# Performance work log

Hardware: AMD Instinct MI355X
Metric: run time of the kernel (lower is better)

Reference implementation:

```python
import jax, jax.numpy as jnp
import numpy as np
from jax import lax

DIM = 256
NH = 16          # num_heads; head_dim = DIM//NH == NH (required by scale broadcast)
HD = DIM // NH   # 16
HID = int(DIM * 1.0)  # mlp hidden (ffn_expansion_factor=1.0)
B, H, W = 4, 128, 128
EPS = 1e-5


def _conv(x, w, pad, groups=1):
    # x: NCHW, w: OIHW
    return lax.conv_general_dilated(x, w, (1, 1), [(pad, pad), (pad, pad)],
                                    dimension_numbers=('NCHW', 'OIHW', 'NCHW'),
                                    feature_group_count=groups)


def _ln(x, w, b):
    # WithBias LayerNorm over channel axis (torch does it in b,(hw),c layout -> axis=c)
    mu = x.mean(1, keepdims=True)
    var = ((x - mu) ** 2).mean(1, keepdims=True)
    return (x - mu) / jnp.sqrt(var + EPS) * w[None, :, None, None] + b[None, :, None, None]


def setup_inputs() -> dict:
    key = jax.random.key(0)
    ks = jax.random.split(key, 12)
    s = 0.02
    return {
        'x': jax.random.normal(ks[0], (B, DIM, H, W), jnp.float32),
        'ln1_w': jnp.ones((DIM,), jnp.float32),
        'ln1_b': jnp.zeros((DIM,), jnp.float32),
        'conv3_w': jax.random.normal(ks[1], (DIM, 1, 3, 3), jnp.float32) * s,
        'conv3_b': jnp.zeros((DIM,), jnp.float32),
        'conv5_w': jax.random.normal(ks[2], (DIM, 1, 5, 5), jnp.float32) * s,
        'conv5_b': jnp.zeros((DIM,), jnp.float32),
        'qkv_w': jax.random.normal(ks[3], (3 * DIM, DIM), jnp.float32) * s,  # 1x1 conv, no bias
        'scale': jnp.ones((NH, 1, 1), jnp.float32),
        'g1_w': jax.random.normal(ks[4], (DIM // 4, DIM), jnp.float32) * s,
        'g1_b': jnp.zeros((DIM // 4,), jnp.float32),
        'g2_w': jax.random.normal(ks[5], (2, DIM // 4), jnp.float32) * s,
        'g2_b': jnp.zeros((2,), jnp.float32),
        'proj_w': jax.random.normal(ks[6], (DIM, DIM), jnp.float32) * s,
        'proj_b': jnp.zeros((DIM,), jnp.float32),
        'ln2_w': jnp.ones((DIM,), jnp.float32),
        'ln2_b': jnp.zeros((DIM,), jnp.float32),
        'pin_w': jax.random.normal(ks[7], (2 * HID, DIM), jnp.float32) * s,  # 1x1, bias=False
        'dw_w': jax.random.normal(ks[8], (2 * HID, 2, 3, 3), jnp.float32) * s,  # groups=HID
        'pout_w': jax.random.normal(ks[9], (DIM, HID), jnp.float32) * s,
    }


def _forward(x, ln1_w, ln1_b, conv3_w, conv3_b, conv5_w, conv5_b, qkv_w, scale,
             g1_w, g1_b, g2_w, g2_b, proj_w, proj_b, ln2_w, ln2_b, pin_w, dw_w, pout_w):
    b, c, h, w = x.shape
    # ---- token mixer (CAFormer) ----
    y = _ln(x, ln1_w, ln1_b)
    conv_feat = (_conv(y, conv3_w, 1, groups=DIM) + conv3_b[None, :, None, None]
                 + _conv(y, conv5_w, 2, groups=DIM) + conv5_b[None, :, None, None])
    qkv = jnp.einsum('oc,bchw->bohw', qkv_w, y)  # (b, 3c, h, w)
    q, k, v = jnp.split(qkv.reshape(b, 3, NH, HD, h * w), 3, axis=1)
    q, k, v = q[:, 0], k[:, 0], v[:, 0]  # (b, nh, hd, h*w)
    # L2 normalize over entire flattened spatial extent (F.normalize, eps=1e-12)
    q = q / jnp.maximum(jnp.linalg.norm(q, axis=-1, keepdims=True), 1e-12)
    k = k / jnp.maximum(jnp.linalg.norm(k, axis=-1, keepdims=True), 1e-12)
    q4 = q.reshape(b, NH, HD, h, w)
    k4 = k.reshape(b, NH, HD, h, w)
    v4 = v.reshape(b, NH, HD, h, w)
    # scale (nh,1,1) right-aligned against (b,nh,hd,x,x): broadcasts along hd axis
    sc = scale.reshape(1, 1, NH, 1, 1)
    # horizontal (row) attention: per (b,head,hd-channel), rows attend to rows
    attn_h = jax.nn.softmax(jnp.einsum('bhdxy,bhdzy->bhdxz', q4, k4) * sc, axis=-1)
    out_h = jnp.einsum('bhdxz,bhdzy->bhdxy', attn_h, v4).reshape(b, c, h, w)
    # vertical (column) attention
    qt, kt, vt = (t.swapaxes(-1, -2) for t in (q4, k4, v4))  # (b,nh,hd,w,h)
    attn_v = jax.nn.softmax(jnp.einsum('bhdyx,bhdzx->bhdyz', qt, kt) * sc, axis=-1)
    out_v = jnp.einsum('bhdyz,bhdzx->bhdyx', attn_v, vt).swapaxes(-1, -2).reshape(b, c, h, w)
    attn_feat = out_h + out_v
    # gate: GAP -> 1x1 -> relu -> 1x1 -> softmax over the 2 branch logits
    gp = y.mean((2, 3))  # (b, c)
    g = jax.nn.relu(gp @ g1_w.T + g1_b)
    g = jax.nn.softmax(g @ g2_w.T + g2_b, axis=-1)  # (b, 2)
    cw = g[:, 0][:, None, None, None]
    aw = g[:, 1][:, None, None, None]
    mixed = cw * conv_feat + aw * attn_feat
    tm = jnp.einsum('oc,bchw->bohw', proj_w, mixed) + proj_b[None, :, None, None]
    x = x + tm
    # ---- MLP ----
    y2 = _ln(x, ln2_w, ln2_b)
    p = jnp.einsum('oc,bchw->bohw', pin_w, y2)  # (b, 2*HID, h, w)
    dwo = _conv(p, dw_w, 1, groups=HID)         # grouped 3x3, 2 ch per group
    x1, x2 = dwo[:, :HID], dwo[:, HID:]
    m = jax.nn.gelu(x1, approximate=False) * x2
    mlp = jnp.einsum('oc,bchw->bohw', pout_w, m)
    return x + mlp


def reference(x, ln1_w, ln1_b, conv3_w, conv3_b, conv5_w, conv5_b, qkv_w, scale,
              g1_w, g1_b, g2_w, g2_b, proj_w, proj_b, ln2_w, ln2_b, pin_w, dw_w, pout_w):
    return _forward(x, ln1_w, ln1_b, conv3_w, conv3_b, conv5_w, conv5_b, qkv_w, scale,
                    g1_w, g1_b, g2_w, g2_b, proj_w, proj_b, ln2_w, ln2_b, pin_w, dw_w, pout_w)
```

## Files before the change

### kernel.cpp

```cpp
#include <hip/hip_runtime.h>
#include <hip/hip_bf16.h>
#include <math.h>

#define DIMC 256
#define NB   4
#define HH   128
#define WW   128
#define HWs  16384
#define HID  256
#define C2   512
#define EPSf 1e-5f

typedef __hip_bfloat16 bf;
typedef unsigned short u16;
typedef unsigned int   u32;
typedef float f32x4  __attribute__((ext_vector_type(4)));
typedef u32   u32x4  __attribute__((ext_vector_type(4)));
typedef short bf16x8 __attribute__((ext_vector_type(8)));

__device__ __forceinline__ float b2f(bf v){ return __bfloat162float(v); }
__device__ __forceinline__ bf    f2b(float v){ return __float2bfloat16(v); }
__device__ __forceinline__ float ldf(const float* p){ return *p; }
__device__ __forceinline__ float ldf(const bf* p){ return __bfloat162float(*p); }
__device__ __forceinline__ void  sto(float* p, float v){ *p = v; }
__device__ __forceinline__ void  sto(bf* p, float v){ *p = f2b(v); }
__device__ __forceinline__ void unpack2(u32 u, float& a, float& b){
  union{u32 x; float f;} lo, hi;
  lo.x = u << 16; hi.x = u & 0xffff0000u;
  a = lo.f; b = hi.f;
}
__device__ __forceinline__ u32 pack2(float a, float b){
  bf h0 = f2b(a), h1 = f2b(b);
  return (u32)*(u16*)&h0 | ((u32)*(u16*)&h1 << 16);
}
__device__ __forceinline__ void unp4(uint2 u, float* d){
  unpack2(u.x, d[0], d[1]); unpack2(u.y, d[2], d[3]);
}

__device__ __forceinline__ float gelu_exact(float v){
  return 0.5f*v*(1.0f + erff(v*0.70710678118654752f));
}

__global__ __launch_bounds__(256) void cvt_all_kernel(
    const float* __restrict__ s0, const float* __restrict__ s1,
    const float* __restrict__ s2, const float* __restrict__ s3,
    u16* __restrict__ d0, u16* __restrict__ d1,
    u16* __restrict__ d2, u16* __restrict__ d3,
    int n0, int n1, int n2, int n3){
  int i = blockIdx.x*256 + threadIdx.x;
  if (i < n0){ bf h = f2b(s0[i]); d0[i] = *(u16*)&h; return; }
  i -= n0;
  if (i < n1){ bf h = f2b(s1[i]); d1[i] = *(u16*)&h; return; }
  i -= n1;
  if (i < n2){ bf h = f2b(s2[i]); d2[i] = *(u16*)&h; return; }
  i -= n2;
  if (i < n3){ bf h = f2b(s3[i]); d3[i] = *(u16*)&h; }
}

__global__ __launch_bounds__(256) void ln_kernel(const float* __restrict__ x,
    const float* __restrict__ w, const float* __restrict__ bb, bf* __restrict__ y){
  int p = blockIdx.x*256 + threadIdx.x;
  int b  = p >> 14;
  int sp = p & (HWs-1);
  const float* xb = x + (size_t)b*DIMC*HWs + sp;
  float s = 0.f, s2 = 0.f;
  for(int c=0;c<DIMC;c++){ float v = xb[(size_t)c*HWs]; s += v; s2 += v*v; }
  float mu   = s * (1.0f/DIMC);
  float var  = s2 * (1.0f/DIMC) - mu*mu;
  float rinv = rsqrtf(var + EPSf);
  bf* yb = y + (size_t)b*DIMC*HWs + sp;
  for(int c=0;c<DIMC;c++){
    float v = xb[(size_t)c*HWs];
    yb[(size_t)c*HWs] = f2b((v - mu)*rinv*w[c] + bb[c]);
  }
}

__global__ __launch_bounds__(256) void ln2px_kernel(const bf* __restrict__ x,
    const float* __restrict__ w, const float* __restrict__ bb, bf* __restrict__ y){
  int p2 = blockIdx.x*256 + threadIdx.x;
  int b  = p2 >> 13;
  int sp = (p2 & 8191) << 1;
  const u16* xb = (const u16*)x + (size_t)b*DIMC*HWs + sp;
  float s0=0.f, s1=0.f, q0=0.f, q1=0.f;
  for(int c=0;c<DIMC;c++){
    u32 u = *(const u32*)(xb + (size_t)c*HWs);
    float a0, a1; unpack2(u, a0, a1);
    s0 += a0; q0 += a0*a0;
    s1 += a1; q1 += a1*a1;
  }
  float mu0 = s0*(1.0f/DIMC), mu1 = s1*(1.0f/DIMC);
  float r0 = rsqrtf(q0*(1.0f/DIMC) - mu0*mu0 + EPSf);
  float r1 = rsqrtf(q1*(1.0f/DIMC) - mu1*mu1 + EPSf);
  u16* yb = (u16*)y + (size_t)b*DIMC*HWs + sp;
  for(int c=0;c<DIMC;c++){
    u32 u = *(const u32*)(xb + (size_t)c*HWs);
    float a0, a1; unpack2(u, a0, a1);
    float wc = w[c], bc = bb[c];
    *(u32*)(yb + (size_t)c*HWs) = pack2((a0-mu0)*r0*wc + bc, (a1-mu1)*r1*wc + bc);
  }
}

__global__ __launch_bounds__(256) void gp_kernel(const bf* __restrict__ y, float* __restrict__ gp){
  int bc = blockIdx.x;
  const u32x4* pl = (const u32x4*)(y + (size_t)bc*HWs);
  float s = 0.f;
  for(int i=threadIdx.x;i<2048;i+=256){
    u32x4 v = pl[i];
    #pragma unroll
    for(int q=0;q<4;q++){
      float a0, a1; unpack2(((const u32*)&v)[q], a0, a1);
      s += a0 + a1;
    }
  }
  __shared__ float red[256];
  red[threadIdx.x] = s; __syncthreads();
  for(int o=128;o>0;o>>=1){
    if(threadIdx.x<o) red[threadIdx.x] += red[threadIdx.x+o];
    __syncthreads();
  }
  if(threadIdx.x==0) gp[bc] = red[0]*(1.0f/HWs);
}

__global__ __launch_bounds__(256) void gate_kernel(const float* __restrict__ gp,
    const float* __restrict__ g1w, const float* __restrict__ g1b,
    const float* __restrict__ g2w, const float* __restrict__ g2b,
    float* __restrict__ cwaw){
  __shared__ float h[NB][64];
  __shared__ float zz[NB][2];
  int t = threadIdx.x;
  int b = t >> 6, j = t & 63;
  const float* gpb = gp + b*DIMC;
  const float* wr  = g1w + j*DIMC;
  float s = g1b[j];
  for(int c=0;c<DIMC;c++) s += gpb[c]*wr[c];
  h[b][j] = fmaxf(s, 0.f);
  __syncthreads();
  if (t < 8){
    int b2 = t >> 1, o = t & 1;
    float z = g2b[o];
    const float* w2 = g2w + o*64;
    for(int q=0;q<64;q++) z += w2[q]*h[b2][q];
    zz[b2][o] = z;
  }
  __syncthreads();
  if (t < 4){
    float z0 = zz[t][0], z1 = zz[t][1];
    float mm = fmaxf(z0,z1);
    float e0 = __expf(z0-mm), e1 = __expf(z1-mm);
    float inv = 1.0f/(e0+e1);
    cwaw[2*t]   = e0*inv;
    cwaw[2*t+1] = e1*inv;
  }
}

__global__ __launch_bounds__(256) void dwconv_kernel(const bf* __restrict__ y,
    const float* __restrict__ w3, const float* __restrict__ b3,
    const float* __restrict__ w5, const float* __restrict__ b5,
    bf* __restrict__ out){
  int bi = blockIdx.x;
  int strip = bi & 7;
  int c  = (bi >> 3) & 255;
  int b  = bi >> 11;
  int t = threadIdx.x;
  int sx = t & 15, ry = t >> 4;
  int hy = strip*16 + ry;
  int x0 = sx << 3;
  const u16* pl = (const u16*)y + ((size_t)(b*DIMC + c))*HWs;

  float kc[25];
  #pragma unroll
  for(int i=0;i<25;i++) kc[i] = w5[c*25+i];
  #pragma unroll
  for(int di=0;di<3;di++)
    #pragma unroll
    for(int dj=0;dj<3;dj++)
      kc[(di+1)*5 + (dj+1)] += w3[c*9 + di*3 + dj];
  float bia = b3[c] + b5[c];

  float acc[8];
  #pragma unroll
  for(int j=0;j<8;j++) acc[j] = bia;

  #pragma unroll
  for(int di=-2; di<=2; di++){
    int yy = hy + di;
    float row[16];
    if ((unsigned)yy < 128u){
      const u16* rp = pl + yy*WW;
      uint2 z; z.x = 0u; z.y = 0u;
      uint2 c0 = (x0 > 0)   ? *(const uint2*)(rp + x0 - 4) : z;
      uint2 c1 = *(const uint2*)(rp + x0);
      uint2 c2 = *(const uint2*)(rp + x0 + 4);
      uint2 c3 = (x0 < 120) ? *(const uint2*)(rp + x0 + 8) : z;
      unp4(c0, row); unp4(c1, row+4); unp4(c2, row+8); unp4(c3, row+12);
    } else {
      #pragma unroll
      for(int j=0;j<16;j++) row[j] = 0.f;
    }
    #pragma unroll
    for(int dj=-2; dj<=2; dj++){
      float w = kc[(di+2)*5 + (dj+2)];
      #pragma unroll
      for(int j=0;j<8;j++) acc[j] += row[4+j+dj]*w;
    }
  }
  u32x4 res;
  #pragma unroll
  for(int q=0;q<4;q++) ((u32*)&res)[q] = pack2(acc[2*q], acc[2*q+1]);
  *(u32x4*)((u16*)out + ((size_t)(b*DIMC + c))*HWs + hy*WW + x0) = res;
}

__global__ __launch_bounds__(256) void dwconv2_glu_kernel(const bf* __restrict__ p,
    const float* __restrict__ w, bf* __restrict__ m){
  int bi = blockIdx.x;
  int strip = bi & 7;
  int op = (bi >> 3) & 127;
  int b  = bi >> 10;
  int o0 = op*2, o1 = o0+1;
  int t = threadIdx.x;
  int sx = t & 15, ry = t >> 4;
  int hy = strip*16 + ry;
  int x0 = sx << 3;
  const u16* p0 = (const u16*)p + ((size_t)b*C2 + o0)*HWs;
  const u16* p1 = p0 + HWs;
  const u16* p2 = p0 + (size_t)256*HWs;
  const u16* p3 = p2 + HWs;

  float KA0[9], KA1[9], KA2[9], KA3[9];
  float KB0[9], KB1[9], KB2[9], KB3[9];
  #pragma unroll
  for(int i=0;i<9;i++){
    KA0[i] = w[o0*18 + i];        KA1[i] = w[o0*18 + 9 + i];
    KA2[i] = w[(o0+256)*18 + i];  KA3[i] = w[(o0+256)*18 + 9 + i];
    KB0[i] = w[o1*18 + i];        KB1[i] = w[o1*18 + 9 + i];
    KB2[i] = w[(o1+256)*18 + i];  KB3[i] = w[(o1+256)*18 + 9 + i];
  }

  float a1A[8] = {}, a2A[8] = {}, a1B[8] = {}, a2B[8] = {};
  #pragma unroll
  for(int di=-1; di<=1; di++){
    int yy = hy + di;
    if ((unsigned)yy >= 128u) continue;
    int roff = yy*WW;
    float r0[16], r1[16], r2[16], r3[16];
    uint2 z; z.x = 0u; z.y = 0u;
    bool lo = (x0 > 0), hi = (x0 < 120);
    {
      const u16* rp = p0 + roff;
      uint2 c0 = lo ? *(const uint2*)(rp + x0 - 4) : z;
      uint2 c1 = *(const uint2*)(rp + x0);
      uint2 c2 = *(const uint2*)(rp + x0 + 4);
      uint2 c3 = hi ? *(const uint2*)(rp + x0 + 8) : z;
      unp4(c0, r0); unp4(c1, r0+4); unp4(c2, r0+8); unp4(c3, r0+12);
    }
    {
      const u16* rp = p1 + roff;
      uint2 c0 = lo ? *(const uint2*)(rp + x0 - 4) : z;
      uint2 c1 = *(const uint2*)(rp + x0);
      uint2 c2 = *(const uint2*)(rp + x0 + 4);
      uint2 c3 = hi ? *(const uint2*)(rp + x0 + 8) : z;
      unp4(c0, r1); unp4(c1, r1+4); unp4(c2, r1+8); unp4(c3, r1+12);
    }
    {
      const u16* rp = p2 + roff;
      uint2 c0 = lo ? *(const uint2*)(rp + x0 - 4) : z;
      uint2 c1 = *(const uint2*)(rp + x0);
      uint2 c2 = *(const uint2*)(rp + x0 + 4);
      uint2 c3 = hi ? *(const uint2*)(rp + x0 + 8) : z;
      unp4(c0, r2); unp4(c1, r2+4); unp4(c2, r2+8); unp4(c3, r2+12);
    }
    {
      const u16* rp = p3 + roff;
      uint2 c0 = lo ? *(const uint2*)(rp + x0 - 4) : z;
      uint2 c1 = *(const uint2*)(rp + x0);
      uint2 c2 = *(const uint2*)(rp + x0 + 4);
      uint2 c3 = hi ? *(const uint2*)(rp + x0 + 8) : z;
      unp4(c0, r3); unp4(c1, r3+4); unp4(c2, r3+8); unp4(c3, r3+12);
    }
    #pragma unroll
    for(int dj=-1; dj<=1; dj++){
      int ki = (di+1)*3 + (dj+1);
      #pragma unroll
      for(int j=0;j<8;j++){
        int ii = 4+j+dj;
        a1A[j] += r0[ii]*KA0[ki] + r1[ii]*KA1[ki];
        a2A[j] += r2[ii]*KA2[ki] + r3[ii]*KA3[ki];
        a1B[j] += r0[ii]*KB0[ki] + r1[ii]*KB1[ki];
        a2B[j] += r2[ii]*KB2[ki] + r3[ii]*KB3[ki];
      }
    }
  }
  size_t obase = ((size_t)(b*DIMC + o0))*HWs + hy*WW + x0;
  u32x4 resA, resB;
  #pragma unroll
  for(int q=0;q<4;q++){
    ((u32*)&resA)[q] = pack2(gelu_exact(a1A[2*q])*a2A[2*q],
                             gelu_exact(a1A[2*q+1])*a2A[2*q+1]);
    ((u32*)&resB)[q] = pack2(gelu_exact(a1B[2*q])*a2B[2*q],
                             gelu_exact(a1B[2*q+1])*a2B[2*q+1]);
  }
  *(u32x4*)((u16*)m + obase) = resA;
  *(u32x4*)((u16*)m + obase + HWs) = resB;
}

template<typename TRES, typename TOUT>
__global__ __launch_bounds__(256, 4) void mfma_gemm(
    const u16* __restrict__ Wb, const bf* __restrict__ act,
    const float* __restrict__ bias, const TRES* __restrict__ resid,
    TOUT* __restrict__ out, int Oc)
{
  __shared__ u16 As[2][4608];
  __shared__ u16 Bs[2][4096];
  int t  = threadIdx.x;
  int n0 = blockIdx.x * 128;
  int o0 = blockIdx.y * 128;
  int b  = n0 >> 14;
  int sp = n0 & (HWs-1);
  const u16* actu = (const u16*)act + (size_t)b*256*HWs + sp;

  int kp = t & 15;
  int ns = (t >> 4) << 3;
  int lane = t & 63;
  int wv = t >> 6;
  int wr = (wv >> 1) << 6;
  int wc = (wv & 1) << 6;
  int fr = lane & 15;
  int kg = lane >> 4;
  int arow = t >> 1;
  int ahalf = (t & 1) << 4;

  f32x4 acc[4][4] = {};

  auto loadB = [&](int ks, u32x4& u, u32x4& v){
    const u16* r0 = actu + (size_t)(ks*32 + 2*kp)*HWs + ns;
    u = *(const u32x4*)r0;
    v = *(const u32x4*)(r0 + HWs);
  };
  auto writeB = [&](const u32x4& u, const u32x4& v, int buf){
    u32 w0=(u.x&0xffffu)|(v.x<<16), w1=(u.x>>16)|(v.x&0xffff0000u);
    u32 w2=(u.y&0xffffu)|(v.y<<16), w3=(u.y>>16)|(v.y&0xffff0000u);
    u32 w4=(u.z&0xffffu)|(v.z<<16), w5=(u.z>>16)|(v.z&0xffff0000u);
    u32 w6=(u.w&0xffffu)|(v.w<<16), w7=(u.w>>16)|(v.w&0xffff0000u);
    u16* bp = Bs[buf];
    int c0 = kp*2;
    *(u32*)&bp[(ns+0)*32+c0]=w0; *(u32*)&bp[(ns+1)*32+c0]=w1;
    *(u32*)&bp[(ns+2)*32+c0]=w2; *(u32*)&bp[(ns+3)*32+c0]=w3;
    *(u32*)&bp[(ns+4)*32+c0]=w4; *(u32*)&bp[(ns+5)*32+c0]=w5;
    *(u32*)&bp[(ns+6)*32+c0]=w6; *(u32*)&bp[(ns+7)*32+c0]=w7;
  };
  auto loadA = [&](int ks, u32x4& a0, u32x4& a1){
    const u16* ap = Wb + (size_t)(o0+arow)*256 + ks*32 + ahalf;
    a0 = *(const u32x4*)ap;
    a1 = *(const u32x4*)(ap + 8);
  };
  auto writeA = [&](const u32x4& a0, const u32x4& a1, int buf){
    u16* dst = &As[buf][arow*36 + ahalf];
    *(u32x4*)dst = a0;
    *(u32x4*)(dst+8) = a1;
  };

  {
    u32x4 bu, bvv, a0, a1;
    loadB(0, bu, bvv); loadA(0, a0, a1);
    writeB(bu, bvv, 0); writeA(a0, a1, 0);
  }
  #pragma unroll
  for(int ks=0; ks<8; ++ks){
    int cur = ks & 1;
    __syncthreads();
    u32x4 bu, bvv, a0, a1;
    if (ks < 7){ loadB(ks+1, bu, bvv); loadA(ks+1, a0, a1); }
    bf16x8 af[4], bfr[4];
    #pragma unroll
    for(int j=0;j<4;j++)
      bfr[j] = *(const bf16x8*)&Bs[cur][(wc + j*16 + fr)*32 + kg*8];
    #pragma unroll
    for(int i=0;i<4;i++)
      af[i] = *(const bf16x8*)&As[cur][(wr + i*16 + fr)*36 + kg*8];
    #pragma unroll
    for(int i=0;i<4;i++)
      #pragma unroll
      for(int j=0;j<4;j++)
        acc[i][j] = __builtin_amdgcn_mfma_f32_16x16x32_bf16(af[i], bfr[j], acc[i][j], 0, 0, 0);
    if (ks < 7){ writeB(bu, bvv, cur^1); writeA(a0, a1, cur^1); }
  }

  #pragma unroll
  for(int i=0;i<4;i++){
    #pragma unroll
    for(int reg=0;reg<4;reg++){
      int o = o0 + wr + i*16 + kg*4 + reg;
      size_t rowoff = ((size_t)b*Oc + o)*HWs + sp + wc + fr;
      float bia = bias ? bias[o] : 0.f;
      #pragma unroll
      for(int j=0;j<4;j++){
        float val = acc[i][j][reg] + bia;
        size_t pidx = rowoff + (size_t)(j*16);
        if (resid) val += ldf(resid + pidx);
        sto(out + pidx, val);
      }
    }
  }
}

#define SWB(r,c2) ((r)*256 + ((c2) ^ ((((r)&7)<<4)) ^ ((((r)>>3)&1)<<6)))

__global__ __launch_bounds__(256, 2) void attn_mfma(const bf* __restrict__ qkv,
    const float* __restrict__ scale, bf* __restrict__ outp,
    const bf* __restrict__ conv, const float* __restrict__ cwaw){
  __shared__ u16 LB0[16384];
  __shared__ u16 LB1[16384];
  __shared__ float2 red2[4];
  int s  = blockIdx.x;
  int b  = s >> 8;
  int ch = s & 255;
  const u16* qp = (const u16*)qkv + ((size_t)b*768 + ch)*HWs;
  const u16* kp = qp + (size_t)256*HWs;
  const u16* vp = qp + (size_t)512*HWs;
  int t = threadIdx.x;

  int lane = t & 63, wvi = t >> 6;
  int fr = lane & 15, kg = lane >> 4;
  int nb = wvi << 5;
  int rr = t >> 1, hb = (t & 1) << 7;
  int kp2 = (t & 15)*2, cs = (t >> 4) << 3;

  auto nat_load = [&](const u16* src, u32x4* R){
    #pragma unroll
    for(int i=0;i<8;i++)
      R[i] = *(const u32x4*)((const char*)src + rr*256 + hb + i*16);
  };
  auto nat_write = [&](const u32x4* R, u16* dst){
    #pragma unroll
    for(int i=0;i<8;i++)
      *(u32x4*)((char*)dst + SWB(rr, hb + i*16)) = R[i];
  };
  auto nat_write_sum = [&](const u32x4* R, u16* dst) -> float {
    float ssum = 0.f;
    #pragma unroll
    for(int i=0;i<8;i++){
      *(u32x4*)((char*)dst + SWB(rr, hb + i*16)) = R[i];
      #pragma unroll
      for(int q=0;q<4;q++){
        float a0, a1;
        unpack2(((const u32*)&R[i])[q], a0, a1);
        ssum += a0*a0 + a1*a1;
      }
    }
    return ssum;
  };
  auto tr_load = [&](const u16* src, u32x4* R){
    #pragma unroll
    for(int bi=0;bi<4;bi++){
      int sr = bi*32 + kp2;
      R[2*bi]   = *(const u32x4*)(src + sr*128 + cs);
      R[2*bi+1] = *(const u32x4*)(src + (sr+1)*128 + cs);
    }
  };
  auto tr_load_lds = [&](const u16* lb, u32x4* R){
    #pragma unroll
    for(int bi=0;bi<4;bi++){
      int sr = bi*32 + kp2;
      R[2*bi]   = *(const u32x4*)((const char*)lb + SWB(sr,   cs*2));
      R[2*bi+1] = *(const u32x4*)((const char*)lb + SWB(sr+1, cs*2));
    }
  };
  auto tr_write = [&](const u32x4* R, u16* dst){
    #pragma unroll
    for(int bi=0;bi<4;bi++){
      int sr = bi*32 + kp2;
      #pragma unroll
      for(int j=0;j<8;j++){
        u32 uw = ((const u32*)&R[2*bi])[j>>1];
        u32 vw = ((const u32*)&R[2*bi+1])[j>>1];
        u32 wv = (j&1) ? ((uw>>16) | (vw & 0xffff0000u))
                       : ((uw & 0xffffu) | (vw<<16));
        *(u32*)((char*)dst + SWB(cs+j, sr*2)) = wv;
      }
    }
  };

  f32x4 acc[8][2];
  f32x4 oacc[8][2];
  const f32x4 vzero = {};
  float ls = 0.f;

  auto mmloop = [&](const u16* afsrc, const u16* bfsrc, f32x4 (&A)[8][2]){
    #pragma unroll
    for(int kk=0;kk<128;kk+=32){
      int kb2 = kk*2 + kg*16;
      bf16x8 b0 = *(const bf16x8*)((const char*)bfsrc + SWB(nb+fr,    kb2));
      bf16x8 b1 = *(const bf16x8*)((const char*)bfsrc + SWB(nb+16+fr, kb2));
      #pragma unroll
      for(int mt=0;mt<8;mt++){
        bf16x8 a0 = *(const bf16x8*)((const char*)afsrc + SWB(mt*16+fr, kb2));
        A[mt][0] = __builtin_amdgcn_mfma_f32_16x16x32_bf16(a0, b0, A[mt][0], 0, 0, 0);
        A[mt][1] = __builtin_amdgcn_mfma_f32_16x16x32_bf16(a0, b1, A[mt][1], 0, 0, 0);
      }
    }
  };

  auto writeCT = [&](u16* dst, f32x4 (&A)[8][2]){
    #pragma unroll
    for(int nt=0;nt<2;nt++){
      int n = nb + nt*16 + fr;
      #pragma unroll
      for(int mt=0;mt<8;mt++){
        #pragma unroll
        for(int pr=0;pr<2;pr++){
          u32 wv = pack2(A[mt][nt][pr*2], A[mt][nt][pr*2+1]);
          int z2 = (mt*16 + kg*4 + pr*2)*2;
          *(u32*)((char*)dst + SWB(n, z2)) = wv;
        }
      }
    }
  };

  auto softmax = [&](){
    #pragma unroll
    for(int nt=0;nt<2;nt++){
      float mx = -1e30f;
      #pragma unroll
      for(int mt=0;mt<8;mt++)
        #pragma unroll
        for(int rg=0;rg<4;rg++){
          acc[mt][nt][rg] *= ls;
          mx = fmaxf(mx, acc[mt][nt][rg]);
        }
      mx = fmaxf(mx, __shfl_xor(mx,16));
      mx = fmaxf(mx, __shfl_xor(mx,32));
      float sm = 0.f;
      #pragma unroll
      for(int mt=0;mt<8;mt++)
        #pragma unroll
        for(int rg=0;rg<4;rg++){
          float e = __expf(acc[mt][nt][rg]-mx);
          acc[mt][nt][rg] = e; sm += e;
        }
      sm += __shfl_xor(sm,16);
      sm += __shfl_xor(sm,32);
      float inv = 1.0f/sm;
      #pragma unroll
      for(int mt=0;mt<8;mt++)
        #pragma unroll
        for(int rg=0;rg<4;rg++)
          acc[mt][nt][rg] *= inv;
    }
  };

  u32x4 RK[8], RQ[8], RV[8];

  nat_load(kp, RK);
  nat_load(qp, RQ);
  tr_load(vp, RV);
  float sk = nat_write_sum(RK, LB0);
  float sq = nat_write_sum(RQ, LB1);
  #pragma unroll
  for(int off=1; off<64; off<<=1){
    sq += __shfl_xor(sq, off);
    sk += __shfl_xor(sk, off);
  }
  if (lane == 0) red2[wvi] = make_float2(sq, sk);
  __syncthreads();
  {
    float tq = 0.f, tk = 0.f;
    #pragma unroll
    for(int wI=0;wI<4;wI++){ tq += red2[wI].x; tk += red2[wI].y; }
    float nq = fmaxf(sqrtf(tq), 1e-12f);
    float nk = fmaxf(sqrtf(tk), 1e-12f);
    ls = scale[ch & 15] / (nq*nk);
  }

  #pragma unroll
  for(int mt=0;mt<8;mt++){ acc[mt][0]=vzero; acc[mt][1]=vzero; }
  mmloop(LB0, LB1, acc);
  softmax();
  tr_load_lds(LB0, RK);
  tr_load_lds(LB1, RQ);
  __syncthreads();

  writeCT(LB0, acc);
  tr_write(RV, LB1);
  __syncthreads();

  #pragma unroll
  for(int mt=0;mt<8;mt++){ oacc[mt][0]=vzero; oacc[mt][1]=vzero; }
  mmloop(LB1, LB0, oacc);
  __syncthreads();

  tr_write(RK, LB0);
  tr_write(RQ, LB1);
  nat_load(vp, RV);
  __syncthreads();

  #pragma unroll
  for(int mt=0;mt<8;mt++){ acc[mt][0]=vzero; acc[mt][1]=vzero; }
  mmloop(LB0, LB1, acc);
  softmax();
  __syncthreads();

  writeCT(LB0, acc);
  nat_write(RV, LB1);
  const u16* cp = (const u16*)conv + ((size_t)b*DIMC + ch)*HWs;
  u32x4 RC[8];
  #pragma unroll
  for(int i=0;i<8;i++)
    RC[i] = *(const u32x4*)(cp + rr*128 + (hb>>1) + i*8);
  __syncthreads();

  mmloop(LB0, LB1, oacc);
  __syncthreads();

  writeCT(LB0, oacc);
  __syncthreads();

  float cw = cwaw[2*b], aw = cwaw[2*b+1];
  bf* op = outp + ((size_t)b*DIMC + ch)*HWs;
  #pragma unroll
  for(int i=0;i<8;i++){
    int c2 = hb + i*16;
    u32x4 ov = *(const u32x4*)((char*)LB0 + SWB(rr, c2));
    u32x4 res;
    #pragma unroll
    for(int q=0;q<4;q++){
      float o0,o1,c0,c1;
      unpack2(((u32*)&ov)[q], o0, o1);
      unpack2(((const u32*)&RC[i])[q], c0, c1);
      ((u32*)&res)[q] = pack2(cw*c0 + aw*o0, cw*c1 + aw*o1);
    }
    *(u32x4*)((u16*)op + rr*128 + (hb>>1) + i*8) = res;
  }
}

extern "C" void kernel_launch(void* const* d_in, const int* in_sizes, int n_in,
                              void* d_out, int out_size, void* d_ws, size_t ws_size,
                              hipStream_t stream){
  (void)in_sizes; (void)n_in; (void)out_size; (void)ws_size;
  const float* x       = (const float*)d_in[0];
  const float* ln1_w   = (const float*)d_in[1];
  const float* ln1_b   = (const float*)d_in[2];
  const float* conv3_w = (const float*)d_in[3];
  const float* conv3_b = (const float*)d_in[4];
  const float* conv5_w = (const float*)d_in[5];
  const float* conv5_b = (const float*)d_in[6];
  const float* qkv_w   = (const float*)d_in[7];
  const float* scale   = (const float*)d_in[8];
  const float* g1_w    = (const float*)d_in[9];
  const float* g1_b    = (const float*)d_in[10];
  const float* g2_w    = (const float*)d_in[11];
  const float* g2_b    = (const float*)d_in[12];
  const float* proj_w  = (const float*)d_in[13];
  const float* proj_b  = (const float*)d_in[14];
  const float* ln2_w   = (const float*)d_in[15];
  const float* ln2_b   = (const float*)d_in[16];
  const float* pin_w   = (const float*)d_in[17];
  const float* dw_w    = (const float*)d_in[18];
  const float* pout_w  = (const float*)d_in[19];
  float* out = (float*)d_out;
  char* wsb  = (char*)d_ws;

  const size_t MB = 1024*1024;
  bf* y    = (bf*)(wsb +   0*MB);
  bf* conv = (bf*)(wsb +  32*MB);
  bf* qkv  = (bf*)(wsb +  64*MB);
  bf* attnf= (bf*)(wsb +   0*MB);
  bf* xnew = (bf*)(wsb +  64*MB);
  bf* y2   = (bf*)(wsb +  96*MB);
  bf* p    = (bf*)(wsb +   0*MB);
  bf* m    = (bf*)(wsb +  96*MB);
  u16* Wqkv  = (u16*)(wsb + 160*MB);
  u16* Wproj = Wqkv + 196608;
  u16* Wpin  = Wproj + 65536;
  u16* Wpout = Wpin + 131072;
  float* gp     = (float*)(Wpout + 65536);
  float* cwaw   = gp + 1024;

  cvt_all_kernel<<<1792,256,0,stream>>>(qkv_w, proj_w, pin_w, pout_w,
                                        Wqkv, Wproj, Wpin, Wpout,
                                        196608, 65536, 131072, 65536);

  ln_kernel<<<256,256,0,stream>>>(x, ln1_w, ln1_b, y);
  gp_kernel<<<1024,256,0,stream>>>(y, gp);
  gate_kernel<<<1,256,0,stream>>>(gp, g1_w, g1_b, g2_w, g2_b, cwaw);
  dwconv_kernel<<<8192,256,0,stream>>>(y, conv3_w, conv3_b, conv5_w, conv5_b, conv);
  mfma_gemm<float,bf><<<dim3(512,6),256,0,stream>>>(Wqkv, y, nullptr,
                                        (const float*)nullptr, qkv, 768);
  attn_mfma<<<1024,256,0,stream>>>(qkv, scale, attnf, conv, cwaw);
  mfma_gemm<float,bf><<<dim3(512,2),256,0,stream>>>(Wproj, attnf, proj_b, x, xnew, 256);
  ln2px_kernel<<<128,256,0,stream>>>(xnew, ln2_w, ln2_b, y2);
  mfma_gemm<float,bf><<<dim3(512,4),256,0,stream>>>(Wpin, y2, nullptr,
                                        (const float*)nullptr, p, 512);
  dwconv2_glu_kernel<<<4096,256,0,stream>>>(p, dw_w, m);
  mfma_gemm<bf,float><<<dim3(512,2),256,0,stream>>>(Wpout, m, nullptr, xnew, out, 256);
}
```

Baseline: 403.8 us.

## Remap GEMM blocks for XCD-aware L2 reuse and vectorize LN1 two pixels per thread

The GEMM grid becomes one-dimensional, and the block index is remapped so that all output-channel tiles of a pixel tile land on the same XCD (consecutive block IDs round-robin across the 8 XCDs). Activation tiles are then reused from that XCD's L2 instead of being fetched by several XCDs. LN1 now handles two pixels per thread with float2 loads and packed bf16 stores, using half the blocks. The LN change halves parallelism, and LN1 uses only 128 blocks, which may underfill the GPU.

```diff
diff --git a/kernel.cpp b/kernel.cpp
--- a/kernel.cpp
+++ b/kernel.cpp
@@ -57,21 +57,26 @@
   if (i < n3){ bf h = f2b(s3[i]); d3[i] = *(u16*)&h; }
 }
 
-__global__ __launch_bounds__(256) void ln_kernel(const float* __restrict__ x,
+__global__ __launch_bounds__(256) void ln1_2px_kernel(const float* __restrict__ x,
     const float* __restrict__ w, const float* __restrict__ bb, bf* __restrict__ y){
-  int p = blockIdx.x*256 + threadIdx.x;
-  int b  = p >> 14;
-  int sp = p & (HWs-1);
+  int p2 = blockIdx.x*256 + threadIdx.x;
+  int b  = p2 >> 13;
+  int sp = (p2 & 8191) << 1;
   const float* xb = x + (size_t)b*DIMC*HWs + sp;
-  float s = 0.f, s2 = 0.f;
-  for(int c=0;c<DIMC;c++){ float v = xb[(size_t)c*HWs]; s += v; s2 += v*v; }
-  float mu   = s * (1.0f/DIMC);
-  float var  = s2 * (1.0f/DIMC) - mu*mu;
-  float rinv = rsqrtf(var + EPSf);
-  bf* yb = y + (size_t)b*DIMC*HWs + sp;
+  float s0=0.f, s1=0.f, q0=0.f, q1=0.f;
   for(int c=0;c<DIMC;c++){
-    float v = xb[(size_t)c*HWs];
-    yb[(size_t)c*HWs] = f2b((v - mu)*rinv*w[c] + bb[c]);
+    float2 v = *(const float2*)(xb + (size_t)c*HWs);
+    s0 += v.x; q0 += v.x*v.x;
+    s1 += v.y; q1 += v.y*v.y;
+  }
+  float mu0 = s0*(1.0f/DIMC), mu1 = s1*(1.0f/DIMC);
+  float r0 = rsqrtf(q0*(1.0f/DIMC) - mu0*mu0 + EPSf);
+  float r1 = rsqrtf(q1*(1.0f/DIMC) - mu1*mu1 + EPSf);
+  u16* yb = (u16*)y + (size_t)b*DIMC*HWs + sp;
+  for(int c=0;c<DIMC;c++){
+    float2 v = *(const float2*)(xb + (size_t)c*HWs);
+    float wc = w[c], bc = bb[c];
+    *(u32*)(yb + (size_t)c*HWs) = pack2((v.x-mu0)*r0*wc + bc, (v.y-mu1)*r1*wc + bc);
   }
 }
 
@@ -303,7 +308,7 @@
   *(u32x4*)((u16*)m + obase + HWs) = resB;
 }
 
-template<typename TRES, typename TOUT>
+template<int NY, typename TRES, typename TOUT>
 __global__ __launch_bounds__(256, 4) void mfma_gemm(
     const u16* __restrict__ Wb, const bf* __restrict__ act,
     const float* __restrict__ bias, const TRES* __restrict__ resid,
@@ -312,8 +317,13 @@
   __shared__ u16 As[2][4608];
   __shared__ u16 Bs[2][4096];
   int t  = threadIdx.x;
-  int n0 = blockIdx.x * 128;
-  int o0 = blockIdx.y * 128;
+  int bid = blockIdx.x;
+  int xcd = bid & 7;
+  int local = bid >> 3;
+  int xg = xcd + 8*(local / NY);
+  int yg = local % NY;
+  int n0 = xg * 128;
+  int o0 = yg * 128;
   int b  = n0 >> 14;
   int sp = n0 & (HWs-1);
   const u16* actu = (const u16*)act + (size_t)b*256*HWs + sp;
@@ -679,17 +689,17 @@
                                         Wqkv, Wproj, Wpin, Wpout,
                                         196608, 65536, 131072, 65536);
 
-  ln_kernel<<<256,256,0,stream>>>(x, ln1_w, ln1_b, y);
+  ln1_2px_kernel<<<128,256,0,stream>>>(x, ln1_w, ln1_b, y);
   gp_kernel<<<1024,256,0,stream>>>(y, gp);
   gate_kernel<<<1,256,0,stream>>>(gp, g1_w, g1_b, g2_w, g2_b, cwaw);
   dwconv_kernel<<<8192,256,0,stream>>>(y, conv3_w, conv3_b, conv5_w, conv5_b, conv);
-  mfma_gemm<float,bf><<<dim3(512,6),256,0,stream>>>(Wqkv, y, nullptr,
+  mfma_gemm<6,float,bf><<<3072,256,0,stream>>>(Wqkv, y, nullptr,
                                         (const float*)nullptr, qkv, 768);
   attn_mfma<<<1024,256,0,stream>>>(qkv, scale, attnf, conv, cwaw);
-  mfma_gemm<float,bf><<<dim3(512,2),256,0,stream>>>(Wproj, attnf, proj_b, x, xnew, 256);
+  mfma_gemm<2,float,bf><<<1024,256,0,stream>>>(Wproj, attnf, proj_b, x, xnew, 256);
   ln2px_kernel<<<128,256,0,stream>>>(xnew, ln2_w, ln2_b, y2);
-  mfma_gemm<float,bf><<<dim3(512,4),256,0,stream>>>(Wpin, y2, nullptr,
+  mfma_gemm<4,float,bf><<<2048,256,0,stream>>>(Wpin, y2, nullptr,
                                         (const float*)nullptr, p, 512);
   dwconv2_glu_kernel<<<4096,256,0,stream>>>(p, dw_w, m);
-  mfma_gemm<bf,float><<<dim3(512,2),256,0,stream>>>(Wpout, m, nullptr, xnew, out, 256);
-}
+  mfma_gemm<2,bf,float><<<1024,256,0,stream>>>(Wpout, m, nullptr, xnew, out, 256);
+}
```

After: 439.0 us. 8.7% more time.
